# Kernel tuning notes

Hardware: AMD Instinct MI355X
Metric: run time of the kernel (lower is better)

Reference implementation:

```python
import jax, jax.numpy as jnp
import numpy as np

GRID = 7          # grid_unit
NSAMPLE = 48      # sample_num
RADIUS = 0.3      # radiu_grid
FEAT = 128


def square_distance(src, dst):
    # src [B,N,C], dst [B,M,C] -> [B,N,M]
    d = -2.0 * jnp.einsum('bnc,bmc->bnm', src, dst)
    d = d + jnp.sum(src * src, -1)[:, :, None]
    d = d + jnp.sum(dst * dst, -1)[:, None, :]
    return d


def batch_norm(x):
    n = jnp.sqrt(jnp.sum(x * x, axis=2, keepdims=True) + 1e-8)
    return x / (n + 1e-10)


def query_ball_point(radius, nsample, xyz, new_xyz):
    B, N, _ = xyz.shape
    sqr = square_distance(new_xyz, xyz)                       # [B,S,N]
    gidx = jnp.where(sqr > radius ** 2, N, jnp.arange(N)[None, None, :])
    gidx = jnp.sort(gidx, axis=-1)[:, :, :nsample]            # [B,S,ns]
    first = gidx[:, :, :1]
    return jnp.where(gidx == N, first, gidx)


def index_points(points, idx):
    # points [B,N,C], idx [B,S,K] -> [B,S,K,C]
    return jax.vmap(lambda p, i: p[i])(points, idx)


def _forward(xyz, pts_feat, W0, b0, W1, b1, W_unet, index):
    B = xyz.shape[0]
    pts = jnp.transpose(xyz[:, 0:3, :], (0, 2, 1))            # [B,N,3]
    N = pts.shape[1]
    g = GRID

    # mlp0 / mlp1 (Conv1d(128,3,1)) + batch_norm
    oris = batch_norm(pts_feat @ W0.T + b0)                   # [B,N,3]
    nors = batch_norm(pts_feat @ W1.T + b1)                   # [B,N,3]

    # ---- rot_pts_3D ----
    gidx = query_ball_point(RADIUS, NSAMPLE, pts, pts)        # [B,N,48]
    group_pts = index_points(pts, gidx)                       # [B,N,48,3]
    group_feat = index_points(pts_feat, gidx).reshape(-1, NSAMPLE, FEAT)  # [BN,48,128]

    ori_rot90 = batch_norm(jnp.cross(oris, nors))
    ori_0 = batch_norm(jnp.cross(ori_rot90, nors))
    rot = jnp.concatenate([ori_0, ori_rot90, nors], axis=-1).reshape(-1, 3, 3)
    rot = jnp.transpose(rot, (0, 2, 1))                       # [BN,3,3]

    local = (group_pts - pts[:, :, None, :]).reshape(-1, NSAMPLE, 3)
    local_pts = jnp.einsum('bsc,bcd->bsd', local, rot)        # [BN,48,3]

    coords = jnp.round((local_pts + RADIUS) / (2 * RADIUS) * (g - 1)).astype(jnp.int32)
    coords = jnp.clip(coords, 0, g - 1)
    # faithful to the original flattening: x*g + y*g + z
    idx = coords[..., 0] * g + coords[..., 1] * g + coords[..., 2]  # [BN,48]

    BN = local_pts.shape[0]
    grid0 = jnp.zeros((BN, g * g * g, FEAT), dtype=pts_feat.dtype)
    feat3d = grid0.at[jnp.arange(BN)[:, None], idx].set(group_feat)  # [BN,343,128]

    # ---- UNet3D stand-in: [BN,128,7,7,7] -> [BN,3,7,7] via (channel,depth) projection
    feat5d = feat3d.reshape(BN, g, g, g, FEAT)
    feat_off = jnp.einsum('bijkc,ckd->bijd', feat5d, W_unet).reshape(BN, g * g, 3)

    # ---- rot_offset ----
    vals = jnp.array([[i * 0.01, j * 0.01, 0.0]
                      for i in range(-30, 36, 10)
                      for j in range(-30, 36, 10)], dtype=pts.dtype)   # [49,3]
    up = vals[None] + feat_off                                # [BN,49,3]
    pts_repeat = pts.reshape(-1, 1, 3)                        # [BN,1,3]
    pts_up = jnp.einsum('bsc,bdc->bsd', up, rot) + pts_repeat  # v @ rot^T

    pts_offset = pts_up[:, 24, :].reshape(B, -1, 3)           # [B,N,3]
    pts_ups = pts_up[:, index, :].reshape(B, -1, 3)           # [B,16N,3]
    return (oris, nors, pts_ups, pts_offset, pts_up)


def setup_inputs() -> dict:
    key = jax.random.key(0)
    ks = jax.random.split(key, 6)
    B, N, C = 2, 1024, 128
    xyz = jax.random.normal(ks[0], (B, 3, N), dtype=jnp.float32)
    pts_feat = jax.random.normal(ks[1], (B, N, C), dtype=jnp.float32)
    W0 = jax.random.normal(ks[2], (3, C), dtype=jnp.float32) * 0.05
    b0 = jnp.zeros((3,), dtype=jnp.float32)
    W1 = jax.random.normal(ks[3], (3, C), dtype=jnp.float32) * 0.05
    b1 = jnp.zeros((3,), dtype=jnp.float32)
    W_unet = jax.random.normal(ks[4], (C, GRID, 3), dtype=jnp.float32) * 0.02
    index = jax.random.randint(ks[5], (16,), 0, GRID * GRID)
    return {"xyz": xyz, "pts_feat": pts_feat, "W0": W0, "b0": b0,
            "W1": W1, "b1": b1, "W_unet": W_unet, "index": index}


def reference(xyz, pts_feat, W0, b0, W1, b1, W_unet, index):
    return _forward(xyz, pts_feat, W0, b0, W1, b1, W_unet, index)
```

## Files before the change

### kernel.cpp

```cpp
#include <hip/hip_runtime.h>

#define NB 2
#define NP 1024
#define NC 128
#define NG 7
#define NSM 48
#define BN (NB*NP)

#define OFF_ORIS 0
#define OFF_NORS (BN*3)
#define OFF_PUPS (2*BN*3)
#define OFF_POFF (OFF_PUPS + BN*16*3)
#define OFF_PU   (OFF_POFF + BN*3)

__device__ __forceinline__ void bnorm3(float v[3]) {
    float ss = __fadd_rn(__fadd_rn(__fmul_rn(v[0],v[0]), __fmul_rn(v[1],v[1])), __fmul_rn(v[2],v[2]));
    float nr = sqrtf(__fadd_rn(ss, 1e-8f));
    float dn = __fadd_rn(nr, 1e-10f);
    v[0] = __fdiv_rn(v[0], dn);
    v[1] = __fdiv_rn(v[1], dn);
    v[2] = __fdiv_rn(v[2], dn);
}

__global__ __launch_bounds__(256) void kfused(const float* __restrict__ xyz,
                                              const float* __restrict__ feat,
                                              const float* __restrict__ W0, const float* __restrict__ b0,
                                              const float* __restrict__ W1, const float* __restrict__ b1,
                                              const float* __restrict__ W_unet,
                                              const int* __restrict__ index,
                                              float* __restrict__ out) {
    __shared__ float srot[9];
    __shared__ unsigned long long smask[16];
    __shared__ int   sgidx[NSM];
    __shared__ int   sidx[NSM];
    __shared__ int   scell[91];
    __shared__ float sfo[NG*NG*3];
    __shared__ float spu[NG*NG*3];

    int p = blockIdx.x;
    int b = p >> 10, n = p & (NP - 1);
    int tid = threadIdx.x;
    int w = tid >> 6, l = tid & 63;
    const float* xb = xyz + (size_t)b*3*NP;

    if (tid < NG*NG*3) sfo[tid] = 0.0f;
    if (tid < 91)      scell[tid] = -1;

    float cx = xb[n], cy = xb[NP + n], cz = xb[2*NP + n];
    float cn = __fadd_rn(__fadd_rn(__fmul_rn(cx,cx), __fmul_rn(cy,cy)), __fmul_rn(cz,cz));

    if (w == 0) {
        float f0 = feat[p*NC + l];
        float f1 = feat[p*NC + 64 + l];
        float s0 = f0*W0[l]     + f1*W0[64+l];
        float s1 = f0*W0[128+l] + f1*W0[192+l];
        float s2 = f0*W0[256+l] + f1*W0[320+l];
        float s3 = f0*W1[l]     + f1*W1[64+l];
        float s4 = f0*W1[128+l] + f1*W1[192+l];
        float s5 = f0*W1[256+l] + f1*W1[320+l];
        for (int off = 32; off; off >>= 1) {
            s0 += __shfl_xor(s0, off);
            s1 += __shfl_xor(s1, off);
            s2 += __shfl_xor(s2, off);
            s3 += __shfl_xor(s3, off);
            s4 += __shfl_xor(s4, off);
            s5 += __shfl_xor(s5, off);
        }
        if (l == 0) {
            float o[3]  = { s0 + b0[0], s1 + b0[1], s2 + b0[2] };
            float nn[3] = { s3 + b1[0], s4 + b1[1], s5 + b1[2] };
            bnorm3(o);
            bnorm3(nn);
            float r90[3];
            r90[0] = __fsub_rn(__fmul_rn(o[1], nn[2]), __fmul_rn(o[2], nn[1]));
            r90[1] = __fsub_rn(__fmul_rn(o[2], nn[0]), __fmul_rn(o[0], nn[2]));
            r90[2] = __fsub_rn(__fmul_rn(o[0], nn[1]), __fmul_rn(o[1], nn[0]));
            bnorm3(r90);
            float o0[3];
            o0[0] = __fsub_rn(__fmul_rn(r90[1], nn[2]), __fmul_rn(r90[2], nn[1]));
            o0[1] = __fsub_rn(__fmul_rn(r90[2], nn[0]), __fmul_rn(r90[0], nn[2]));
            o0[2] = __fsub_rn(__fmul_rn(r90[0], nn[1]), __fmul_rn(r90[1], nn[0]));
            bnorm3(o0);

            out[OFF_ORIS + p*3+0] = o[0];  out[OFF_ORIS + p*3+1] = o[1];  out[OFF_ORIS + p*3+2] = o[2];
            out[OFF_NORS + p*3+0] = nn[0]; out[OFF_NORS + p*3+1] = nn[1]; out[OFF_NORS + p*3+2] = nn[2];

            srot[0] = o0[0];  srot[1] = o0[1];  srot[2] = o0[2];
            srot[3] = r90[0]; srot[4] = r90[1]; srot[5] = r90[2];
            srot[6] = nn[0];  srot[7] = nn[1];  srot[8] = nn[2];
        }
        {
            int m = l;
            float mx = xb[m], my = xb[NP + m], mz = xb[2*NP + m];
            float mn = __fadd_rn(__fadd_rn(__fmul_rn(mx,mx), __fmul_rn(my,my)), __fmul_rn(mz,mz));
            float dot = __fadd_rn(__fadd_rn(__fmul_rn(cx,mx), __fmul_rn(cy,my)), __fmul_rn(cz,mz));
            float d = __fadd_rn(__fadd_rn(__fmul_rn(-2.0f, dot), cn), mn);
            unsigned long long mk = __ballot(!(d > 0.09f));
            if (l == 0) smask[0] = mk;
        }
    } else {
        int ch0 = (w - 1) * 5 + 1;
        #pragma unroll
        for (int k = 0; k < 5; ++k) {
            int ch = ch0 + k;
            int m = (ch << 6) + l;
            float mx = xb[m], my = xb[NP + m], mz = xb[2*NP + m];
            float mn = __fadd_rn(__fadd_rn(__fmul_rn(mx,mx), __fmul_rn(my,my)), __fmul_rn(mz,mz));
            float dot = __fadd_rn(__fadd_rn(__fmul_rn(cx,mx), __fmul_rn(cy,my)), __fmul_rn(cz,mz));
            float d = __fadd_rn(__fadd_rn(__fmul_rn(-2.0f, dot), cn), mn);
            unsigned long long mk = __ballot(!(d > 0.09f));
            if (l == 0) smask[ch] = mk;
        }
    }
    __syncthreads();

    if (tid < 16) {
        unsigned long long wv = smask[tid];
        int prefix = 0, total = 0, firstj = 0;
        bool seen = false;
        #pragma unroll
        for (int j = 0; j < 16; ++j) {
            int pc = __popcll(smask[j]);
            if (j < tid) prefix += pc;
            if (!seen && pc) { firstj = j; seen = true; }
            total += pc;
        }
        int pos = prefix;
        while (wv && pos < NSM) {
            int bpos = __ffsll(wv) - 1;
            sgidx[pos++] = (tid << 6) + bpos;
            wv &= wv - 1;
        }
        if (total < NSM) {
            int first = (firstj << 6) + (__ffsll(smask[firstj]) - 1);
            for (int q2 = total + tid; q2 < NSM; q2 += 16) sgidx[q2] = first;
        }
    }
    __syncthreads();

    if (tid < NSM) {
        int m = sgidx[tid];
        float lx = __fsub_rn(xb[m],        cx);
        float ly = __fsub_rn(xb[NP + m],   cy);
        float lz = __fsub_rn(xb[2*NP + m], cz);
        int c[3];
        #pragma unroll
        for (int dd = 0; dd < 3; ++dd) {
            float lp = __fadd_rn(__fadd_rn(__fmul_rn(lx, srot[dd*3+0]),
                                           __fmul_rn(ly, srot[dd*3+1])),
                                 __fmul_rn(lz, srot[dd*3+2]));
            float t = rintf(__fmul_rn(__fdiv_rn(__fadd_rn(lp, 0.3f), 0.6f), 6.0f));
            int ci = (int)t;
            ci = ci < 0 ? 0 : (ci > 6 ? 6 : ci);
            c[dd] = ci;
        }
        int cell = c[0]*NG + c[1]*NG + c[2];
        sidx[tid] = cell;
        atomicMax(&scell[cell], tid);
    }
    __syncthreads();

    {
        int sl = tid & 15;
        int sg = tid >> 4;
        #pragma unroll
        for (int r = 0; r < 3; ++r) {
            int s = r*16 + sg;
            int cell = sidx[s];
            if (scell[cell] == s) {
                int k = cell % NG;
                int q = cell / NG;
                const float* fr = feat + (size_t)(b*NP + sgidx[s]) * NC;
                float p0 = 0.f, p1 = 0.f, p2 = 0.f;
                #pragma unroll
                for (int c8 = 0; c8 < 8; ++c8) {
                    int cc = sl + c8*16;
                    float f = fr[cc];
                    const float* wp = W_unet + cc*(NG*3) + k*3;
                    p0 += f * wp[0];
                    p1 += f * wp[1];
                    p2 += f * wp[2];
                }
                #pragma unroll
                for (int off = 8; off; off >>= 1) {
                    p0 += __shfl_xor(p0, off);
                    p1 += __shfl_xor(p1, off);
                    p2 += __shfl_xor(p2, off);
                }
                if (sl == 0) {
                    atomicAdd(&sfo[q*3+0], p0);
                    atomicAdd(&sfo[q*3+1], p1);
                    atomicAdd(&sfo[q*3+2], p2);
                }
            }
        }
    }
    __syncthreads();

    if (tid < NG*NG*3) {
        int q = tid / 3, d = tid % 3;
        int qi = q / NG, qj = q % NG;
        float v0 = (float)((-30 + 10*qi) * 0.01);
        float v1 = (float)((-30 + 10*qj) * 0.01);
        float u0 = __fadd_rn(v0, sfo[q*3+0]);
        float u1 = __fadd_rn(v1, sfo[q*3+1]);
        float u2 = sfo[q*3+2];
        float ctr = (d == 0) ? cx : (d == 1) ? cy : cz;
        float r = __fadd_rn(
                    __fadd_rn(
                      __fadd_rn(__fmul_rn(u0, srot[0*3+d]), __fmul_rn(u1, srot[1*3+d])),
                      __fmul_rn(u2, srot[2*3+d])),
                    ctr);
        spu[tid] = r;
        out[OFF_PU + p*(NG*NG*3) + tid] = r;
        if (q == 24) out[OFF_POFF + p*3 + d] = r;
    }
    __syncthreads();

    if (tid < 16*3) {
        int t = tid / 3, d = tid % 3;
        int q = index[t];
        out[OFF_PUPS + (p*16 + t)*3 + d] = spu[q*3 + d];
    }
}

extern "C" void kernel_launch(void* const* d_in, const int* in_sizes, int n_in,
                              void* d_out, int out_size, void* d_ws, size_t ws_size,
                              hipStream_t stream) {
    const float* xyz    = (const float*)d_in[0];
    const float* feat   = (const float*)d_in[1];
    const float* W0     = (const float*)d_in[2];
    const float* b0     = (const float*)d_in[3];
    const float* W1     = (const float*)d_in[4];
    const float* b1     = (const float*)d_in[5];
    const float* W_unet = (const float*)d_in[6];
    const int*   index  = (const int*)d_in[7];
    float* out = (float*)d_out;

    hipLaunchKernelGGL(kfused, dim3(BN), dim3(256), 0, stream,
                       xyz, feat, W0, b0, W1, b1, W_unet, index, out);
}
```

Measured before the change: 78.70 us.

## Collapse per-point block to a single wavefront with early-exit ball query

Shrinks each block from four wavefronts to one 64-thread wavefront. The frame math is computed redundantly in every lane and kept in registers instead of shared memory. The ball query now scans chunks in order, compacting selected neighbours with ballot and popcount, and stops as soon as 48 neighbours are found. The winner-cell feature projections are processed serially across the wave with shuffles, so shared-memory atomics and several barriers go away. The cost is less parallelism per point and serialized cell projections in exchange for less synchronization and skipped distance work.

```diff
diff --git a/kernel.cpp b/kernel.cpp
--- a/kernel.cpp
+++ b/kernel.cpp
@@ -13,212 +13,166 @@
 #define OFF_POFF (OFF_PUPS + BN*16*3)
 #define OFF_PU   (OFF_POFF + BN*3)
 
-__device__ __forceinline__ void bnorm3(float v[3]) {
-    float ss = __fadd_rn(__fadd_rn(__fmul_rn(v[0],v[0]), __fmul_rn(v[1],v[1])), __fmul_rn(v[2],v[2]));
-    float nr = sqrtf(__fadd_rn(ss, 1e-8f));
-    float dn = __fadd_rn(nr, 1e-10f);
-    v[0] = __fdiv_rn(v[0], dn);
-    v[1] = __fdiv_rn(v[1], dn);
-    v[2] = __fdiv_rn(v[2], dn);
-}
+#define BN3(x,y,z) do { \
+    float ss = __fadd_rn(__fadd_rn(__fmul_rn(x,x), __fmul_rn(y,y)), __fmul_rn(z,z)); \
+    float nr = sqrtf(__fadd_rn(ss, 1e-8f)); \
+    float dn = __fadd_rn(nr, 1e-10f); \
+    x = __fdiv_rn(x, dn); y = __fdiv_rn(y, dn); z = __fdiv_rn(z, dn); \
+} while (0)
 
-__global__ __launch_bounds__(256) void kfused(const float* __restrict__ xyz,
-                                              const float* __restrict__ feat,
-                                              const float* __restrict__ W0, const float* __restrict__ b0,
-                                              const float* __restrict__ W1, const float* __restrict__ b1,
-                                              const float* __restrict__ W_unet,
-                                              const int* __restrict__ index,
-                                              float* __restrict__ out) {
-    __shared__ float srot[9];
-    __shared__ unsigned long long smask[16];
+__global__ __launch_bounds__(64) void kfused(const float* __restrict__ xyz,
+                                             const float* __restrict__ feat,
+                                             const float* __restrict__ W0, const float* __restrict__ b0,
+                                             const float* __restrict__ W1, const float* __restrict__ b1,
+                                             const float* __restrict__ W_unet,
+                                             const int* __restrict__ index,
+                                             float* __restrict__ out) {
     __shared__ int   sgidx[NSM];
-    __shared__ int   sidx[NSM];
     __shared__ int   scell[91];
     __shared__ float sfo[NG*NG*3];
     __shared__ float spu[NG*NG*3];
 
     int p = blockIdx.x;
     int b = p >> 10, n = p & (NP - 1);
-    int tid = threadIdx.x;
-    int w = tid >> 6, l = tid & 63;
+    int l = threadIdx.x;
     const float* xb = xyz + (size_t)b*3*NP;
 
-    if (tid < NG*NG*3) sfo[tid] = 0.0f;
-    if (tid < 91)      scell[tid] = -1;
+    scell[l] = -1;
+    if (l + 64 < 91) scell[l + 64] = -1;
+    sfo[l] = 0.0f; sfo[l + 64] = 0.0f;
+    if (l + 128 < NG*NG*3) sfo[l + 128] = 0.0f;
 
     float cx = xb[n], cy = xb[NP + n], cz = xb[2*NP + n];
     float cn = __fadd_rn(__fadd_rn(__fmul_rn(cx,cx), __fmul_rn(cy,cy)), __fmul_rn(cz,cz));
 
-    if (w == 0) {
-        float f0 = feat[p*NC + l];
-        float f1 = feat[p*NC + 64 + l];
-        float s0 = f0*W0[l]     + f1*W0[64+l];
-        float s1 = f0*W0[128+l] + f1*W0[192+l];
-        float s2 = f0*W0[256+l] + f1*W0[320+l];
-        float s3 = f0*W1[l]     + f1*W1[64+l];
-        float s4 = f0*W1[128+l] + f1*W1[192+l];
-        float s5 = f0*W1[256+l] + f1*W1[320+l];
+    float f0 = feat[p*NC + l];
+    float f1 = feat[p*NC + 64 + l];
+    float s0 = f0*W0[l]     + f1*W0[64+l];
+    float s1 = f0*W0[128+l] + f1*W0[192+l];
+    float s2 = f0*W0[256+l] + f1*W0[320+l];
+    float s3 = f0*W1[l]     + f1*W1[64+l];
+    float s4 = f0*W1[128+l] + f1*W1[192+l];
+    float s5 = f0*W1[256+l] + f1*W1[320+l];
+    for (int off = 32; off; off >>= 1) {
+        s0 += __shfl_xor(s0, off);
+        s1 += __shfl_xor(s1, off);
+        s2 += __shfl_xor(s2, off);
+        s3 += __shfl_xor(s3, off);
+        s4 += __shfl_xor(s4, off);
+        s5 += __shfl_xor(s5, off);
+    }
+    float ox = s0 + b0[0], oy = s1 + b0[1], oz = s2 + b0[2];
+    float nx = s3 + b1[0], ny = s4 + b1[1], nz = s5 + b1[2];
+    BN3(ox, oy, oz);
+    BN3(nx, ny, nz);
+    float rx = __fsub_rn(__fmul_rn(oy, nz), __fmul_rn(oz, ny));
+    float ry = __fsub_rn(__fmul_rn(oz, nx), __fmul_rn(ox, nz));
+    float rz = __fsub_rn(__fmul_rn(ox, ny), __fmul_rn(oy, nx));
+    BN3(rx, ry, rz);
+    float ax = __fsub_rn(__fmul_rn(ry, nz), __fmul_rn(rz, ny));
+    float ay = __fsub_rn(__fmul_rn(rz, nx), __fmul_rn(rx, nz));
+    float az = __fsub_rn(__fmul_rn(rx, ny), __fmul_rn(ry, nx));
+    BN3(ax, ay, az);
+    if (l == 0) {
+        out[OFF_ORIS + p*3+0] = ox; out[OFF_ORIS + p*3+1] = oy; out[OFF_ORIS + p*3+2] = oz;
+        out[OFF_NORS + p*3+0] = nx; out[OFF_NORS + p*3+1] = ny; out[OFF_NORS + p*3+2] = nz;
+    }
+
+    int count = 0, first = -1;
+    for (int ch = 0; ch < 16 && count < NSM; ++ch) {
+        int m = (ch << 6) + l;
+        float mx = xb[m], my = xb[NP + m], mz = xb[2*NP + m];
+        float mn = __fadd_rn(__fadd_rn(__fmul_rn(mx,mx), __fmul_rn(my,my)), __fmul_rn(mz,mz));
+        float dot = __fadd_rn(__fadd_rn(__fmul_rn(cx,mx), __fmul_rn(cy,my)), __fmul_rn(cz,mz));
+        float d = __fadd_rn(__fadd_rn(__fmul_rn(-2.0f, dot), cn), mn);
+        bool sel = !(d > 0.09f);
+        unsigned long long mk = __ballot(sel);
+        if (first < 0 && mk != 0ull) first = (ch << 6) + (__ffsll(mk) - 1);
+        if (sel) {
+            int pos = count + (int)__popcll(mk & ((1ull << l) - 1ull));
+            if (pos < NSM) sgidx[pos] = m;
+        }
+        count += (int)__popcll(mk);
+    }
+    __syncthreads();
+    if (count < NSM) {
+        for (int i2 = count + l; i2 < NSM; i2 += 64) sgidx[i2] = first;
+    }
+    __syncthreads();
+
+    int cell = 0, msamp = 0;
+    if (l < NSM) {
+        msamp = sgidx[l];
+        float lx = __fsub_rn(xb[msamp],        cx);
+        float ly = __fsub_rn(xb[NP + msamp],   cy);
+        float lz = __fsub_rn(xb[2*NP + msamp], cz);
+        float lp0 = __fadd_rn(__fadd_rn(__fmul_rn(lx, ax), __fmul_rn(ly, ay)), __fmul_rn(lz, az));
+        float lp1 = __fadd_rn(__fadd_rn(__fmul_rn(lx, rx), __fmul_rn(ly, ry)), __fmul_rn(lz, rz));
+        float lp2 = __fadd_rn(__fadd_rn(__fmul_rn(lx, nx), __fmul_rn(ly, ny)), __fmul_rn(lz, nz));
+        float t0 = rintf(__fmul_rn(__fdiv_rn(__fadd_rn(lp0, 0.3f), 0.6f), 6.0f));
+        float t1 = rintf(__fmul_rn(__fdiv_rn(__fadd_rn(lp1, 0.3f), 0.6f), 6.0f));
+        float t2 = rintf(__fmul_rn(__fdiv_rn(__fadd_rn(lp2, 0.3f), 0.6f), 6.0f));
+        int c0 = (int)t0; c0 = c0 < 0 ? 0 : (c0 > 6 ? 6 : c0);
+        int c1 = (int)t1; c1 = c1 < 0 ? 0 : (c1 > 6 ? 6 : c1);
+        int c2 = (int)t2; c2 = c2 < 0 ? 0 : (c2 > 6 ? 6 : c2);
+        cell = c0*NG + c1*NG + c2;
+        atomicMax(&scell[cell], l);
+    }
+    __syncthreads();
+
+    bool winner = (l < NSM) && (scell[cell] == l);
+    unsigned long long wmask = __ballot(winner);
+    while (wmask) {
+        int s = __ffsll(wmask) - 1;
+        wmask &= wmask - 1;
+        int cs = __shfl(cell, s);
+        int ms = __shfl(msamp, s);
+        int k = cs % NG, q = cs / NG;
+        const float* fr = feat + (size_t)(b*NP + ms) * NC;
+        const float* w0p = W_unet + l*(NG*3) + k*3;
+        const float* w1p = W_unet + (64+l)*(NG*3) + k*3;
+        float g0 = fr[l], g1 = fr[64+l];
+        float p0 = g0*w0p[0] + g1*w1p[0];
+        float p1 = g0*w0p[1] + g1*w1p[1];
+        float p2 = g0*w0p[2] + g1*w1p[2];
         for (int off = 32; off; off >>= 1) {
-            s0 += __shfl_xor(s0, off);
-            s1 += __shfl_xor(s1, off);
-            s2 += __shfl_xor(s2, off);
-            s3 += __shfl_xor(s3, off);
-            s4 += __shfl_xor(s4, off);
-            s5 += __shfl_xor(s5, off);
+            p0 += __shfl_xor(p0, off);
+            p1 += __shfl_xor(p1, off);
+            p2 += __shfl_xor(p2, off);
         }
         if (l == 0) {
-            float o[3]  = { s0 + b0[0], s1 + b0[1], s2 + b0[2] };
-            float nn[3] = { s3 + b1[0], s4 + b1[1], s5 + b1[2] };
-            bnorm3(o);
-            bnorm3(nn);
-            float r90[3];
-            r90[0] = __fsub_rn(__fmul_rn(o[1], nn[2]), __fmul_rn(o[2], nn[1]));
-            r90[1] = __fsub_rn(__fmul_rn(o[2], nn[0]), __fmul_rn(o[0], nn[2]));
-            r90[2] = __fsub_rn(__fmul_rn(o[0], nn[1]), __fmul_rn(o[1], nn[0]));
-            bnorm3(r90);
-            float o0[3];
-            o0[0] = __fsub_rn(__fmul_rn(r90[1], nn[2]), __fmul_rn(r90[2], nn[1]));
-            o0[1] = __fsub_rn(__fmul_rn(r90[2], nn[0]), __fmul_rn(r90[0], nn[2]));
-            o0[2] = __fsub_rn(__fmul_rn(r90[0], nn[1]), __fmul_rn(r90[1], nn[0]));
-            bnorm3(o0);
-
-            out[OFF_ORIS + p*3+0] = o[0];  out[OFF_ORIS + p*3+1] = o[1];  out[OFF_ORIS + p*3+2] = o[2];
-            out[OFF_NORS + p*3+0] = nn[0]; out[OFF_NORS + p*3+1] = nn[1]; out[OFF_NORS + p*3+2] = nn[2];
-
-            srot[0] = o0[0];  srot[1] = o0[1];  srot[2] = o0[2];
-            srot[3] = r90[0]; srot[4] = r90[1]; srot[5] = r90[2];
-            srot[6] = nn[0];  srot[7] = nn[1];  srot[8] = nn[2];
-        }
-        {
-            int m = l;
-            float mx = xb[m], my = xb[NP + m], mz = xb[2*NP + m];
-            float mn = __fadd_rn(__fadd_rn(__fmul_rn(mx,mx), __fmul_rn(my,my)), __fmul_rn(mz,mz));
-            float dot = __fadd_rn(__fadd_rn(__fmul_rn(cx,mx), __fmul_rn(cy,my)), __fmul_rn(cz,mz));
-            float d = __fadd_rn(__fadd_rn(__fmul_rn(-2.0f, dot), cn), mn);
-            unsigned long long mk = __ballot(!(d > 0.09f));
-            if (l == 0) smask[0] = mk;
-        }
-    } else {
-        int ch0 = (w - 1) * 5 + 1;
-        #pragma unroll
-        for (int k = 0; k < 5; ++k) {
-            int ch = ch0 + k;
-            int m = (ch << 6) + l;
-            float mx = xb[m], my = xb[NP + m], mz = xb[2*NP + m];
-            float mn = __fadd_rn(__fadd_rn(__fmul_rn(mx,mx), __fmul_rn(my,my)), __fmul_rn(mz,mz));
-            float dot = __fadd_rn(__fadd_rn(__fmul_rn(cx,mx), __fmul_rn(cy,my)), __fmul_rn(cz,mz));
-            float d = __fadd_rn(__fadd_rn(__fmul_rn(-2.0f, dot), cn), mn);
-            unsigned long long mk = __ballot(!(d > 0.09f));
-            if (l == 0) smask[ch] = mk;
+            sfo[q*3+0] += p0;
+            sfo[q*3+1] += p1;
+            sfo[q*3+2] += p2;
         }
     }
     __syncthreads();
 
-    if (tid < 16) {
-        unsigned long long wv = smask[tid];
-        int prefix = 0, total = 0, firstj = 0;
-        bool seen = false;
-        #pragma unroll
-        for (int j = 0; j < 16; ++j) {
-            int pc = __popcll(smask[j]);
-            if (j < tid) prefix += pc;
-            if (!seen && pc) { firstj = j; seen = true; }
-            total += pc;
-        }
-        int pos = prefix;
-        while (wv && pos < NSM) {
-            int bpos = __ffsll(wv) - 1;
-            sgidx[pos++] = (tid << 6) + bpos;
-            wv &= wv - 1;
-        }
-        if (total < NSM) {
-            int first = (firstj << 6) + (__ffsll(smask[firstj]) - 1);
-            for (int q2 = total + tid; q2 < NSM; q2 += 16) sgidx[q2] = first;
-        }
-    }
-    __syncthreads();
-
-    if (tid < NSM) {
-        int m = sgidx[tid];
-        float lx = __fsub_rn(xb[m],        cx);
-        float ly = __fsub_rn(xb[NP + m],   cy);
-        float lz = __fsub_rn(xb[2*NP + m], cz);
-        int c[3];
-        #pragma unroll
-        for (int dd = 0; dd < 3; ++dd) {
-            float lp = __fadd_rn(__fadd_rn(__fmul_rn(lx, srot[dd*3+0]),
-                                           __fmul_rn(ly, srot[dd*3+1])),
-                                 __fmul_rn(lz, srot[dd*3+2]));
-            float t = rintf(__fmul_rn(__fdiv_rn(__fadd_rn(lp, 0.3f), 0.6f), 6.0f));
-            int ci = (int)t;
-            ci = ci < 0 ? 0 : (ci > 6 ? 6 : ci);
-            c[dd] = ci;
-        }
-        int cell = c[0]*NG + c[1]*NG + c[2];
-        sidx[tid] = cell;
-        atomicMax(&scell[cell], tid);
-    }
-    __syncthreads();
-
-    {
-        int sl = tid & 15;
-        int sg = tid >> 4;
-        #pragma unroll
-        for (int r = 0; r < 3; ++r) {
-            int s = r*16 + sg;
-            int cell = sidx[s];
-            if (scell[cell] == s) {
-                int k = cell % NG;
-                int q = cell / NG;
-                const float* fr = feat + (size_t)(b*NP + sgidx[s]) * NC;
-                float p0 = 0.f, p1 = 0.f, p2 = 0.f;
-                #pragma unroll
-                for (int c8 = 0; c8 < 8; ++c8) {
-                    int cc = sl + c8*16;
-                    float f = fr[cc];
-                    const float* wp = W_unet + cc*(NG*3) + k*3;
-                    p0 += f * wp[0];
-                    p1 += f * wp[1];
-                    p2 += f * wp[2];
-                }
-                #pragma unroll
-                for (int off = 8; off; off >>= 1) {
-                    p0 += __shfl_xor(p0, off);
-                    p1 += __shfl_xor(p1, off);
-                    p2 += __shfl_xor(p2, off);
-                }
-                if (sl == 0) {
-                    atomicAdd(&sfo[q*3+0], p0);
-                    atomicAdd(&sfo[q*3+1], p1);
-                    atomicAdd(&sfo[q*3+2], p2);
-                }
-            }
-        }
-    }
-    __syncthreads();
-
-    if (tid < NG*NG*3) {
-        int q = tid / 3, d = tid % 3;
-        int qi = q / NG, qj = q % NG;
+    for (int t = l; t < NG*NG*3; t += 64) {
+        int q = t / 3, d = t - q*3;
+        int qi = q / NG, qj = q - qi*NG;
         float v0 = (float)((-30 + 10*qi) * 0.01);
         float v1 = (float)((-30 + 10*qj) * 0.01);
         float u0 = __fadd_rn(v0, sfo[q*3+0]);
         float u1 = __fadd_rn(v1, sfo[q*3+1]);
         float u2 = sfo[q*3+2];
+        float r0d = (d == 0) ? ax : (d == 1) ? ay : az;
+        float r1d = (d == 0) ? rx : (d == 1) ? ry : rz;
+        float r2d = (d == 0) ? nx : (d == 1) ? ny : nz;
         float ctr = (d == 0) ? cx : (d == 1) ? cy : cz;
         float r = __fadd_rn(
                     __fadd_rn(
-                      __fadd_rn(__fmul_rn(u0, srot[0*3+d]), __fmul_rn(u1, srot[1*3+d])),
-                      __fmul_rn(u2, srot[2*3+d])),
+                      __fadd_rn(__fmul_rn(u0, r0d), __fmul_rn(u1, r1d)),
+                      __fmul_rn(u2, r2d)),
                     ctr);
-        spu[tid] = r;
-        out[OFF_PU + p*(NG*NG*3) + tid] = r;
+        spu[t] = r;
+        out[OFF_PU + p*(NG*NG*3) + t] = r;
         if (q == 24) out[OFF_POFF + p*3 + d] = r;
     }
     __syncthreads();
 
-    if (tid < 16*3) {
-        int t = tid / 3, d = tid % 3;
+    if (l < 16*3) {
+        int t = l / 3, d = l - t*3;
         int q = index[t];
         out[OFF_PUPS + (p*16 + t)*3 + d] = spu[q*3 + d];
     }
@@ -237,6 +191,6 @@
     const int*   index  = (const int*)d_in[7];
     float* out = (float*)d_out;
 
-    hipLaunchKernelGGL(kfused, dim3(BN), dim3(256), 0, stream,
+    hipLaunchKernelGGL(kfused, dim3(BN), dim3(64), 0, stream,
                        xyz, feat, W0, b0, W1, b1, W_unet, index, out);
 }
```

Result: slower. 81.32 us (+3.3%).
